# Kernel optimization log

Hardware: AMD Instinct MI355X
Metric: run time of the kernel (lower is better)

The kernel has to match this reference:

```python
import jax, jax.numpy as jnp
import numpy as np

TEMPERATURE = 0.5
EPS = 1e-20


def setup_inputs() -> dict:
    key = jax.random.key(0)
    ks = jax.random.split(key, 7)
    N, T, S = 16, 64, 1024
    SRC, TGT, D = 512, 512, 64
    return {
        "input": jax.random.normal(ks[0], (N, T, TGT), jnp.float32),
        "memory_bank": jax.random.normal(ks[1], (N, S, SRC), jnp.float32),
        "W_q": jax.random.normal(ks[2], (TGT, D), jnp.float32) / np.sqrt(TGT),
        "W_ctx": jax.random.normal(ks[3], (SRC, D), jnp.float32) / np.sqrt(SRC),
        "v": jax.random.normal(ks[4], (D,), jnp.float32) / np.sqrt(D),
        "W_out": jax.random.normal(ks[5], (SRC + TGT, TGT), jnp.float32) / np.sqrt(SRC + TGT),
        "b_out": jax.random.normal(ks[6], (TGT,), jnp.float32) * 0.01,
    }


def reference(input, memory_bank, W_q, W_ctx, v, W_out, b_out):
    # MLP attention score: v^T tanh(W_q q + W_ctx h)
    wq = jnp.einsum("ntd,de->nte", input, W_q)            # [N,T,D]
    uh = jnp.einsum("nsd,de->nse", memory_bank, W_ctx)    # [N,S,D]
    wquh = jnp.tanh(wq[:, :, None, :] + uh[:, None, :, :])  # [N,T,S,D]
    scores = jnp.einsum("ntsd,d->nts", wquh, v)           # [N,T,S]

    log_alpha = jax.nn.log_softmax(scores, axis=-1)
    alpha = jnp.exp(log_alpha)                            # c_align_vectors

    # deterministic context + output
    context_c = jnp.einsum("nts,nsd->ntd", alpha, memory_bank)
    h_c = jnp.tanh(jnp.concatenate([input, context_c], axis=-1) @ W_out + b_out)

    # gumbel-softmax sample (K = n_samples = 1, forced by view_as in original)
    u = jax.random.uniform(jax.random.key(42), log_alpha.shape, jnp.float32)
    g = -jnp.log(-jnp.log(u + EPS) + EPS)                 # gumbel noise
    y_align = jax.nn.softmax((log_alpha + g) / TEMPERATURE, axis=-1)  # [N,T,S]

    context_y = jnp.einsum("nts,nsd->ntd", y_align, memory_bank)
    h_y = jnp.tanh(jnp.concatenate([input, context_y], axis=-1) @ W_out + b_out)

    return jnp.stack([h_c, h_y], axis=0)  # [2,N,T,tgt_dim]
```

## Files before the change

kernel.cpp:

```cpp
#include <hip/hip_runtime.h>
#include <hip/hip_bf16.h>
#include <stdint.h>

#define DEV __device__ __forceinline__

typedef __attribute__((ext_vector_type(8))) short short8;
typedef __attribute__((ext_vector_type(4))) float f32x4;

#define TWO_LOG2E 2.8853900817779268f
#define MFMA16(a, b, c) __builtin_amdgcn_mfma_f32_16x16x32_bf16((a), (b), (c), 0, 0, 0)

DEV unsigned short f2bf(float f) {
  uint32_t u = __float_as_uint(f);
  u += 0x7FFFu + ((u >> 16) & 1u);
  return (unsigned short)(u >> 16);
}

DEV uint2 pk4(float4 f) {
  union { __hip_bfloat162 h; unsigned u; } a, b;
  a.h = __float22bfloat162_rn(make_float2(f.x, f.y));
  b.h = __float22bfloat162_rn(make_float2(f.z, f.w));
  return make_uint2(a.u, b.u);
}

DEV short8 mk8(uint2 lo, uint2 hi) {
  union { short8 s; uint4 u; } t;
  t.u = make_uint4(lo.x, lo.y, hi.x, hi.y);
  return t.s;
}

DEV uint32_t rotl32(uint32_t x, int r) { return (x << r) | (x >> (32 - r)); }

DEV void threefry_0_42(uint32_t x0, uint32_t x1, uint32_t& o0, uint32_t& o1) {
  const uint32_t ks0 = 0u, ks1 = 42u, ks2 = 0x1BD11BDAu ^ 42u;
  x0 += ks0; x1 += ks1;
#define TFR(r) { x0 += x1; x1 = rotl32(x1, (r)); x1 ^= x0; }
  TFR(13) TFR(15) TFR(26) TFR(6)  x0 += ks1; x1 += ks2 + 1u;
  TFR(17) TFR(29) TFR(16) TFR(24) x0 += ks2; x1 += ks0 + 2u;
  TFR(13) TFR(15) TFR(26) TFR(6)  x0 += ks0; x1 += ks1 + 3u;
  TFR(17) TFR(29) TFR(16) TFR(24) x0 += ks1; x1 += ks2 + 4u;
  TFR(13) TFR(15) TFR(26) TFR(6)  x0 += ks2; x1 += ks0 + 5u;
#undef TFR
  o0 = x0; o1 = x1;
}

DEV float wredmax(float v) {
#pragma unroll
  for (int off = 32; off > 0; off >>= 1) v = fmaxf(v, __shfl_xor(v, off));
  return v;
}
DEV float wredsum(float v) {
#pragma unroll
  for (int off = 32; off > 0; off >>= 1) v += __shfl_xor(v, off);
  return v;
}

__global__ __launch_bounds__(256) void k_prep(const float* __restrict__ Wctx,
                                              const float* __restrict__ Wq,
                                              const float* __restrict__ Wout,
                                              unsigned short* __restrict__ WctxT,
                                              unsigned short* __restrict__ WqT,
                                              unsigned short* __restrict__ WoutT) {
  __shared__ float tile[64][65];
  const int b = blockIdx.x;
  const float* src; unsigned short* dst; int R, C, br, bc;
  if (b < 8)       { src = Wctx; dst = WctxT; R = 512;  C = 64;  br = b * 64;       bc = 0; }
  else if (b < 16) { src = Wq;   dst = WqT;   R = 512;  C = 64;  br = (b - 8) * 64; bc = 0; }
  else { int i = b - 16; src = Wout; dst = WoutT; R = 1024; C = 512; br = (i & 15) * 64; bc = (i >> 4) * 64; }
  const int tid = threadIdx.x;
  const int lr = tid >> 4, lc4 = (tid & 15) * 4;
#pragma unroll
  for (int i = 0; i < 4; ++i) {
    float4 vv = *(const float4*)(src + (long)(br + lr + i * 16) * C + bc + lc4);
    tile[lr + i * 16][lc4 + 0] = vv.x;
    tile[lr + i * 16][lc4 + 1] = vv.y;
    tile[lr + i * 16][lc4 + 2] = vv.z;
    tile[lr + i * 16][lc4 + 3] = vv.w;
  }
  __syncthreads();
#pragma unroll
  for (int i = 0; i < 4; ++i) {
    int crow = lr + i * 16;
    ushort4 o;
    o.x = f2bf(tile[lc4 + 0][crow]);
    o.y = f2bf(tile[lc4 + 1][crow]);
    o.z = f2bf(tile[lc4 + 2][crow]);
    o.w = f2bf(tile[lc4 + 3][crow]);
    *(ushort4*)(dst + (long)(bc + crow) * R + br + lc4) = o;
  }
}

__global__ __launch_bounds__(256) void k_gemm1(const float* __restrict__ mb,
                                               const float* __restrict__ input,
                                               const unsigned short* __restrict__ WctxT,
                                               const unsigned short* __restrict__ WqT,
                                               const unsigned short* __restrict__ WoutT,
                                               const float* __restrict__ bout,
                                               float* __restrict__ uhT,
                                               float* __restrict__ wqo,
                                               float* __restrict__ P,
                                               unsigned short* __restrict__ mbT) {
  __shared__ __align__(16) unsigned short As[64][32];
  __shared__ __align__(16) unsigned short Bs[64][32];
  __shared__ __align__(16) unsigned short Tr[32][72];
  const int tid = threadIdx.x;
  const int t = blockIdx.x;
  const int srow = tid >> 2, kc = tid & 3;
  const int scol = ((kc ^ (srow & 3)) * 8);
  const int wave = tid >> 6, lane = tid & 63;
  const int q = lane >> 4, r = lane & 15;
  const int c0 = ((q ^ (r & 3)) * 8);

  if (t < 272) {
    const bool domb = (t < 256);
    const float* A; const unsigned short* BT; int mbase;
    if (domb) { A = mb;    BT = WctxT; mbase = t * 64; }
    else      { A = input; BT = WqT;   mbase = (t - 256) * 64; }
    const int n = mbase >> 10, s0 = mbase & 1023;
    const int wm = (wave >> 1) * 32, wn = (wave & 1) * 32;
    const float* ap = A + (long)(mbase + srow) * 512 + kc * 8;
    const unsigned short* bp = BT + (long)srow * 512 + kc * 8;
    const int trow = tid >> 3, toff = (tid & 7) * 8;
    f32x4 acc[2][2];
#pragma unroll
    for (int i = 0; i < 2; ++i)
#pragma unroll
      for (int j = 0; j < 2; ++j) acc[i][j] = (f32x4){0.f, 0.f, 0.f, 0.f};
    float4 fa0 = *(const float4*)(ap);
    float4 fa1 = *(const float4*)(ap + 4);
    uint4 fb = *(const uint4*)(bp);
    for (int k0 = 0; k0 < 512; k0 += 32) {
      uint2 p0 = pk4(fa0), p1 = pk4(fa1);
      *(uint4*)&As[srow][scol] = make_uint4(p0.x, p0.y, p1.x, p1.y);
      *(uint4*)&Bs[srow][scol] = fb;
      if (domb) {
        const int d0 = kc * 8;
        Tr[d0 + 0][srow] = (unsigned short)(p0.x & 0xFFFFu);
        Tr[d0 + 1][srow] = (unsigned short)(p0.x >> 16);
        Tr[d0 + 2][srow] = (unsigned short)(p0.y & 0xFFFFu);
        Tr[d0 + 3][srow] = (unsigned short)(p0.y >> 16);
        Tr[d0 + 4][srow] = (unsigned short)(p1.x & 0xFFFFu);
        Tr[d0 + 5][srow] = (unsigned short)(p1.x >> 16);
        Tr[d0 + 6][srow] = (unsigned short)(p1.y & 0xFFFFu);
        Tr[d0 + 7][srow] = (unsigned short)(p1.y >> 16);
      }
      __syncthreads();
      if (k0 + 32 < 512) {
        fa0 = *(const float4*)(ap + k0 + 32);
        fa1 = *(const float4*)(ap + k0 + 36);
        fb = *(const uint4*)(bp + k0 + 32);
      }
      short8 a0 = *(const short8*)&As[wm + r][c0];
      short8 a1 = *(const short8*)&As[wm + 16 + r][c0];
      short8 b0 = *(const short8*)&Bs[wn + r][c0];
      short8 b1 = *(const short8*)&Bs[wn + 16 + r][c0];
      acc[0][0] = MFMA16(a0, b0, acc[0][0]);
      acc[0][1] = MFMA16(a0, b1, acc[0][1]);
      acc[1][0] = MFMA16(a1, b0, acc[1][0]);
      acc[1][1] = MFMA16(a1, b1, acc[1][1]);
      if (domb) {
        ushort4 w0 = *(const ushort4*)&Tr[trow][toff];
        ushort4 w1 = *(const ushort4*)&Tr[trow][toff + 4];
        unsigned short* dst = mbT + (long)n * 524288 + (long)(k0 + trow) * 1024 + s0 + toff;
        *(ushort4*)(dst) = w0;
        *(ushort4*)(dst + 4) = w1;
      }
      __syncthreads();
    }
#pragma unroll
    for (int i2 = 0; i2 < 2; ++i2)
#pragma unroll
      for (int j2 = 0; j2 < 2; ++j2) {
        int gcol = wn + j2 * 16 + r;
        int m = mbase + wm + i2 * 16 + q * 4;
        if (domb) {
          int nn = m >> 10, ss = m & 1023;
          float4 o;
          o.x = acc[i2][j2][0] * TWO_LOG2E;
          o.y = acc[i2][j2][1] * TWO_LOG2E;
          o.z = acc[i2][j2][2] * TWO_LOG2E;
          o.w = acc[i2][j2][3] * TWO_LOG2E;
          *(float4*)(uhT + (long)nn * 65536 + (long)gcol * 1024 + ss) = o;
        } else {
#pragma unroll
          for (int reg = 0; reg < 4; ++reg)
            wqo[(long)(m + reg) * 64 + gcol] = acc[i2][j2][reg] * TWO_LOG2E;
        }
      }
  } else {
    const int tt = t - 272;
    const int mbase = (tt >> 4) * 64, nbase = (tt & 15) * 32;
    const int wm = (wave >> 1) * 32, wn = (wave & 1) * 16;
    const float* ap = input + (long)(mbase + srow) * 512 + kc * 8;
    const int brow = (tid & 127) >> 2;
    const unsigned short* bp = WoutT + (long)(nbase + brow) * 1024 + kc * 8;
    f32x4 acc[2];
    acc[0] = (f32x4){0.f, 0.f, 0.f, 0.f};
    acc[1] = (f32x4){0.f, 0.f, 0.f, 0.f};
    float4 fa0 = *(const float4*)(ap);
    float4 fa1 = *(const float4*)(ap + 4);
    uint4 fb;
    if (tid < 128) fb = *(const uint4*)(bp);
    for (int k0 = 0; k0 < 512; k0 += 32) {
      uint2 p0 = pk4(fa0), p1 = pk4(fa1);
      *(uint4*)&As[srow][scol] = make_uint4(p0.x, p0.y, p1.x, p1.y);
      if (tid < 128) *(uint4*)&Bs[brow][(kc ^ (brow & 3)) * 8] = fb;
      __syncthreads();
      int kn = k0 + 32;
      if (kn < 512) {
        fa0 = *(const float4*)(ap + kn);
        fa1 = *(const float4*)(ap + kn + 4);
        if (tid < 128) fb = *(const uint4*)(bp + kn);
      }
      short8 a0 = *(const short8*)&As[wm + r][c0];
      short8 a1 = *(const short8*)&As[wm + 16 + r][c0];
      short8 b0 = *(const short8*)&Bs[wn + r][c0];
      acc[0] = MFMA16(a0, b0, acc[0]);
      acc[1] = MFMA16(a1, b0, acc[1]);
      __syncthreads();
    }
#pragma unroll
    for (int i2 = 0; i2 < 2; ++i2) {
      int gcol = nbase + wn + r;
      float bb = bout[gcol];
#pragma unroll
      for (int reg = 0; reg < 4; ++reg) {
        int grow = mbase + wm + i2 * 16 + q * 4 + reg;
        P[(long)grow * 512 + gcol] = acc[i2][reg] + bb;
      }
    }
  }
}

DEV void softmax_gumbel_write(float* lsc, int nt, int tid, float* red,
                              unsigned short* alpha_bf, unsigned short* yal_bf) {
  const int wv = tid >> 6, ln = tid & 63;
  float m = fmaxf(fmaxf(lsc[0], lsc[1]), fmaxf(lsc[2], lsc[3]));
  m = wredmax(m);
  if (ln == 0) red[wv] = m;
  __syncthreads();
  m = fmaxf(fmaxf(red[0], red[1]), fmaxf(red[2], red[3]));
  __syncthreads();
  float ss = 0.f;
#pragma unroll
  for (int i = 0; i < 4; ++i) ss += __expf(lsc[i] - m);
  ss = wredsum(ss);
  if (ln == 0) red[wv] = ss;
  __syncthreads();
  ss = red[0] + red[1] + red[2] + red[3];
  const float logl = __logf(ss);
  __syncthreads();

  const uint32_t jbase = (uint32_t)nt * 1024u + (uint32_t)tid * 4u;
  float ys[4];
  float4 av;
#pragma unroll
  for (int i = 0; i < 4; ++i) {
    float la = lsc[i] - m - logl;
    ((float*)&av)[i] = __expf(la);
    uint32_t o0, o1;
    threefry_0_42(0u, jbase + i, o0, o1);
    uint32_t bits = o0 ^ o1;
    float u = __uint_as_float((bits >> 9) | 0x3f800000u) - 1.0f;
    float g = -__logf(-__logf(u + 1e-20f) + 1e-20f);
    ys[i] = (la + g) * 2.0f;
  }
  {
    uint2 pa = pk4(av);
    *(uint2*)(alpha_bf + (long)nt * 1024 + tid * 4) = pa;
  }
  float m2 = fmaxf(fmaxf(ys[0], ys[1]), fmaxf(ys[2], ys[3]));
  m2 = wredmax(m2);
  if (ln == 0) red[wv] = m2;
  __syncthreads();
  m2 = fmaxf(fmaxf(red[0], red[1]), fmaxf(red[2], red[3]));
  __syncthreads();
  float s2 = 0.f;
  float4 ye;
#pragma unroll
  for (int i = 0; i < 4; ++i) { ((float*)&ye)[i] = __expf(ys[i] - m2); s2 += ((float*)&ye)[i]; }
  s2 = wredsum(s2);
  if (ln == 0) red[wv] = s2;
  __syncthreads();
  s2 = red[0] + red[1] + red[2] + red[3];
  const float rinv = __fdividef(1.f, s2);
  ye.x *= rinv; ye.y *= rinv; ye.z *= rinv; ye.w *= rinv;
  {
    uint2 py = pk4(ye);
    *(uint2*)(yal_bf + (long)nt * 1024 + tid * 4) = py;
  }
  __syncthreads();
}

__global__ __launch_bounds__(256) void k_scores(const float* __restrict__ uhT,
                                                const float* __restrict__ wqo,
                                                const float* __restrict__ vvec,
                                                unsigned short* __restrict__ alpha_bf,
                                                unsigned short* __restrict__ yal_bf) {
  __shared__ __align__(16) float smf[196];
  float* wvs0 = smf;
  float* wvs1 = smf + 64;
  float* vvs  = smf + 128;
  float* red  = smf + 192;
  const int tid = threadIdx.x;
  const int bid = blockIdx.x;
  const int nt0 = ((bid & 7) << 6) | (bid >> 3);
  const int nt1 = nt0 + 512;
  const int n0 = nt0 >> 6, n1 = nt1 >> 6;
  if (tid < 64) {
    wvs0[tid] = wqo[nt0 * 64 + tid];
    wvs1[tid] = wqo[nt1 * 64 + tid];
    vvs[tid]  = vvec[tid];
  }
  __syncthreads();
  float sumv = 0.f;
#pragma unroll
  for (int d = 0; d < 64; d += 4) {
    float4 vv = *(const float4*)&vvs[d];
    sumv += vv.x + vv.y + vv.z + vv.w;
  }
  const float* un0 = uhT + (long)n0 * 65536 + tid * 4;
  const float* un1 = uhT + (long)n1 * 65536 + tid * 4;
  float4 r0 = make_float4(0.f, 0.f, 0.f, 0.f);
  float4 r1 = make_float4(0.f, 0.f, 0.f, 0.f);
  for (int db = 0; db < 64; db += 4) {
    float4 ua[4], ub[4];
#pragma unroll
    for (int j = 0; j < 4; ++j) {
      ua[j] = *(const float4*)(un0 + (long)(db + j) * 1024);
      ub[j] = *(const float4*)(un1 + (long)(db + j) * 1024);
    }
#pragma unroll
    for (int j = 0; j < 4; ++j) {
      float w0 = wvs0[db + j], w1 = wvs1[db + j], vvj = vvs[db + j];
      r0.x = fmaf(vvj, __builtin_amdgcn_rcpf(1.f + __builtin_amdgcn_exp2f(ua[j].x + w0)), r0.x);
      r0.y = fmaf(vvj, __builtin_amdgcn_rcpf(1.f + __builtin_amdgcn_exp2f(ua[j].y + w0)), r0.y);
      r0.z = fmaf(vvj, __builtin_amdgcn_rcpf(1.f + __builtin_amdgcn_exp2f(ua[j].z + w0)), r0.z);
      r0.w = fmaf(vvj, __builtin_amdgcn_rcpf(1.f + __builtin_amdgcn_exp2f(ua[j].w + w0)), r0.w);
      r1.x = fmaf(vvj, __builtin_amdgcn_rcpf(1.f + __builtin_amdgcn_exp2f(ub[j].x + w1)), r1.x);
      r1.y = fmaf(vvj, __builtin_amdgcn_rcpf(1.f + __builtin_amdgcn_exp2f(ub[j].y + w1)), r1.y);
      r1.z = fmaf(vvj, __builtin_amdgcn_rcpf(1.f + __builtin_amdgcn_exp2f(ub[j].z + w1)), r1.z);
      r1.w = fmaf(vvj, __builtin_amdgcn_rcpf(1.f + __builtin_amdgcn_exp2f(ub[j].w + w1)), r1.w);
    }
  }
  float lsc0[4], lsc1[4];
  lsc0[0] = fmaf(-2.f, r0.x, sumv); lsc0[1] = fmaf(-2.f, r0.y, sumv);
  lsc0[2] = fmaf(-2.f, r0.z, sumv); lsc0[3] = fmaf(-2.f, r0.w, sumv);
  lsc1[0] = fmaf(-2.f, r1.x, sumv); lsc1[1] = fmaf(-2.f, r1.y, sumv);
  lsc1[2] = fmaf(-2.f, r1.z, sumv); lsc1[3] = fmaf(-2.f, r1.w, sumv);
  softmax_gumbel_write(lsc0, nt0, tid, red, alpha_bf, yal_bf);
  softmax_gumbel_write(lsc1, nt1, tid, red, alpha_bf, yal_bf);
}

__global__ __launch_bounds__(256) void k_ctx(const unsigned short* __restrict__ alpha_bf,
                                             const unsigned short* __restrict__ yal_bf,
                                             const unsigned short* __restrict__ mbT,
                                             unsigned short* __restrict__ ctxb) {
  __shared__ __align__(16) unsigned short As[64][32];
  const int tid = threadIdx.x;
  const int x = blockIdx.x;
  const int n = x & 15, dbase = ((x >> 4) & 15) * 32, vt = x >> 8;
  const int srow = tid >> 2, kc = tid & 3;
  const int scol = ((kc ^ (srow & 3)) * 8);
  const int wave = tid >> 6, lane = tid & 63;
  const int wm = (wave >> 1) * 32, wn = (wave & 1) * 16;
  const int q = lane >> 4, r = lane & 15;
  const int c0 = ((q ^ (r & 3)) * 8);
  const unsigned short* Ab = (vt ? yal_bf : alpha_bf) + (long)n * 65536 + (long)srow * 1024 + kc * 8;
  const unsigned short* Bp = mbT + (long)n * 524288 + (long)(dbase + wn + r) * 1024 + q * 8;
  f32x4 acc[2];
  acc[0] = (f32x4){0.f, 0.f, 0.f, 0.f};
  acc[1] = (f32x4){0.f, 0.f, 0.f, 0.f};
  uint4 fa  = *(const uint4*)(Ab);
  uint4 fb0 = *(const uint4*)(Bp);
  uint4 fb1 = *(const uint4*)(Bp + 32);
  for (int k0 = 0; k0 < 1024; k0 += 32) {
    *(uint4*)&As[srow][scol] = fa;
    __syncthreads();
    union { uint4 u; short8 s; } bu; bu.u = fb0;
    if (k0 + 32 < 1024) fa = *(const uint4*)(Ab + k0 + 32);
    fb0 = fb1;
    if (k0 + 64 < 1024) fb1 = *(const uint4*)(Bp + k0 + 64);
    short8 a0 = *(const short8*)&As[wm + r][c0];
    short8 a1 = *(const short8*)&As[wm + 16 + r][c0];
    acc[0] = MFMA16(a0, bu.s, acc[0]);
    acc[1] = MFMA16(a1, bu.s, acc[1]);
    __syncthreads();
  }
#pragma unroll
  for (int i2 = 0; i2 < 2; ++i2) {
    int gcol = dbase + wn + r;
#pragma unroll
    for (int reg = 0; reg < 4; ++reg) {
      long grow = (long)vt * 1024 + n * 64 + wm + i2 * 16 + q * 4 + reg;
      ctxb[grow * 512 + gcol] = f2bf(acc[i2][reg]);
    }
  }
}

__global__ __launch_bounds__(256) void k_out(const unsigned short* __restrict__ ctxb,
                                             const unsigned short* __restrict__ WoutT,
                                             const float* __restrict__ P,
                                             float* __restrict__ out) {
  __shared__ __align__(16) unsigned short As[64][32];
  __shared__ __align__(16) unsigned short Bs[32][32];
  const int tid = threadIdx.x;
  const int mbase = (blockIdx.x >> 4) * 64, nbase = (blockIdx.x & 15) * 32;
  const int srow = tid >> 2, kc = tid & 3;
  const int scol = ((kc ^ (srow & 3)) * 8);
  const int wave = tid >> 6, lane = tid & 63;
  const int wm = (wave >> 1) * 32, wn = (wave & 1) * 16;
  const int q = lane >> 4, r = lane & 15;
  const int c0 = ((q ^ (r & 3)) * 8);
  const unsigned short* ap = ctxb + (long)(mbase + srow) * 512 + kc * 8;
  const int brow = (tid & 127) >> 2;
  const unsigned short* bp = WoutT + (long)(nbase + brow) * 1024 + 512 + kc * 8;
  f32x4 acc[2];
#pragma unroll
  for (int i2 = 0; i2 < 2; ++i2) {
    int pcol = nbase + wn + r;
#pragma unroll
    for (int reg = 0; reg < 4; ++reg) {
      int prow = (mbase + wm + i2 * 16 + q * 4 + reg) & 1023;
      acc[i2][reg] = P[(long)prow * 512 + pcol];
    }
  }
  uint4 fa = *(const uint4*)(ap);
  uint4 fb;
  if (tid < 128) fb = *(const uint4*)(bp);
  for (int k0 = 0; k0 < 512; k0 += 32) {
    *(uint4*)&As[srow][scol] = fa;
    if (tid < 128) *(uint4*)&Bs[brow][(kc ^ (brow & 3)) * 8] = fb;
    __syncthreads();
    int kn = k0 + 32;
    if (kn < 512) {
      fa = *(const uint4*)(ap + kn);
      if (tid < 128) fb = *(const uint4*)(bp + kn);
    }
    short8 a0 = *(const short8*)&As[wm + r][c0];
    short8 a1 = *(const short8*)&As[wm + 16 + r][c0];
    short8 b0 = *(const short8*)&Bs[wn + r][c0];
    acc[0] = MFMA16(a0, b0, acc[0]);
    acc[1] = MFMA16(a1, b0, acc[1]);
    __syncthreads();
  }
#pragma unroll
  for (int i2 = 0; i2 < 2; ++i2) {
    int gcol = nbase + wn + r;
#pragma unroll
    for (int reg = 0; reg < 4; ++reg) {
      int grow = mbase + wm + i2 * 16 + q * 4 + reg;
      float z = acc[i2][reg];
      float rc = __builtin_amdgcn_rcpf(1.f + __builtin_amdgcn_exp2f(z * TWO_LOG2E));
      out[(long)grow * 512 + gcol] = fmaf(-2.f, rc, 1.f);
    }
  }
}

extern "C" void kernel_launch(void* const* d_in, const int* in_sizes, int n_in,
                              void* d_out, int out_size, void* d_ws, size_t ws_size,
                              hipStream_t stream) {
  const float* input = (const float*)d_in[0];
  const float* mb    = (const float*)d_in[1];
  const float* W_q   = (const float*)d_in[2];
  const float* W_ctx = (const float*)d_in[3];
  const float* v     = (const float*)d_in[4];
  const float* W_out = (const float*)d_in[5];
  const float* b_out = (const float*)d_in[6];
  float* out = (float*)d_out;
  float* ws = (float*)d_ws;

  float* uhT = ws;
  float* wqo = ws + 1048576;
  unsigned short* alpha_bf = (unsigned short*)(ws + 1114112);
  unsigned short* yal_bf   = (unsigned short*)(ws + 1638400);
  unsigned short* WctxT = (unsigned short*)(ws + 2162688);
  unsigned short* WqT   = (unsigned short*)(ws + 2179072);
  unsigned short* WoutT = (unsigned short*)(ws + 2195456);
  unsigned short* ctxb  = (unsigned short*)(ws + 2457600);
  float* P = ws + 2981888;
  unsigned short* mbT = (unsigned short*)(ws + 3506176);

  k_prep<<<144, 256, 0, stream>>>(W_ctx, W_q, W_out, WctxT, WqT, WoutT);
  k_gemm1<<<528, 256, 0, stream>>>(mb, input, WctxT, WqT, WoutT, b_out, uhT, wqo, P, mbT);
  k_scores<<<512, 256, 0, stream>>>(uhT, wqo, v, alpha_bf, yal_bf);
  k_ctx<<<512, 256, 0, stream>>>(alpha_bf, yal_bf, mbT, ctxb);
  k_out<<<512, 256, 0, stream>>>(ctxb, WoutT, P, out);
}
```

Measured before the change: 153.1 us.

## Halve per-block tile sizes to double grid size across all GEMM and score kernels

Every kernel is re-tiled so each block handles half as much work: the gemm1 M-tile drops from 64 to 32 rows, k_scores handles one query row per block instead of two, and k_ctx and k_out use 32-row tiles. Grids double from roughly 512 to roughly 1024 blocks, which gives the MI355X's many CUs more blocks to schedule and better latency hiding. In exchange each block reuses less data, so B operands are loaded more often, and half the threads now sit idle during A staging. The transpose tile is reshaped to match, and an unused helper and a trailing barrier are removed.

```diff
diff --git a/kernel.cpp b/kernel.cpp
--- a/kernel.cpp
+++ b/kernel.cpp
@@ -21,12 +21,6 @@
   a.h = __float22bfloat162_rn(make_float2(f.x, f.y));
   b.h = __float22bfloat162_rn(make_float2(f.z, f.w));
   return make_uint2(a.u, b.u);
-}
-
-DEV short8 mk8(uint2 lo, uint2 hi) {
-  union { short8 s; uint4 u; } t;
-  t.u = make_uint4(lo.x, lo.y, hi.x, hi.y);
-  return t.s;
 }
 
 DEV uint32_t rotl32(uint32_t x, int r) { return (x << r) | (x >> (32 - r)); }
@@ -100,134 +94,128 @@
                                                float* __restrict__ wqo,
                                                float* __restrict__ P,
                                                unsigned short* __restrict__ mbT) {
-  __shared__ __align__(16) unsigned short As[64][32];
+  __shared__ __align__(16) unsigned short As[32][32];
   __shared__ __align__(16) unsigned short Bs[64][32];
-  __shared__ __align__(16) unsigned short Tr[32][72];
+  __shared__ __align__(16) unsigned short Tr[32][33];
   const int tid = threadIdx.x;
   const int t = blockIdx.x;
-  const int srow = tid >> 2, kc = tid & 3;
-  const int scol = ((kc ^ (srow & 3)) * 8);
   const int wave = tid >> 6, lane = tid & 63;
   const int q = lane >> 4, r = lane & 15;
   const int c0 = ((q ^ (r & 3)) * 8);
 
-  if (t < 272) {
-    const bool domb = (t < 256);
+  if (t < 544) {
+    const bool domb = (t < 512);
     const float* A; const unsigned short* BT; int mbase;
-    if (domb) { A = mb;    BT = WctxT; mbase = t * 64; }
-    else      { A = input; BT = WqT;   mbase = (t - 256) * 64; }
+    if (domb) { A = mb;    BT = WctxT; mbase = t * 32; }
+    else      { A = input; BT = WqT;   mbase = (t - 512) * 32; }
     const int n = mbase >> 10, s0 = mbase & 1023;
-    const int wm = (wave >> 1) * 32, wn = (wave & 1) * 32;
-    const float* ap = A + (long)(mbase + srow) * 512 + kc * 8;
-    const unsigned short* bp = BT + (long)srow * 512 + kc * 8;
-    const int trow = tid >> 3, toff = (tid & 7) * 8;
-    f32x4 acc[2][2];
-#pragma unroll
-    for (int i = 0; i < 2; ++i)
-#pragma unroll
-      for (int j = 0; j < 2; ++j) acc[i][j] = (f32x4){0.f, 0.f, 0.f, 0.f};
-    float4 fa0 = *(const float4*)(ap);
-    float4 fa1 = *(const float4*)(ap + 4);
-    uint4 fb = *(const uint4*)(bp);
-    for (int k0 = 0; k0 < 512; k0 += 32) {
-      uint2 p0 = pk4(fa0), p1 = pk4(fa1);
-      *(uint4*)&As[srow][scol] = make_uint4(p0.x, p0.y, p1.x, p1.y);
-      *(uint4*)&Bs[srow][scol] = fb;
-      if (domb) {
-        const int d0 = kc * 8;
-        Tr[d0 + 0][srow] = (unsigned short)(p0.x & 0xFFFFu);
-        Tr[d0 + 1][srow] = (unsigned short)(p0.x >> 16);
-        Tr[d0 + 2][srow] = (unsigned short)(p0.y & 0xFFFFu);
-        Tr[d0 + 3][srow] = (unsigned short)(p0.y >> 16);
-        Tr[d0 + 4][srow] = (unsigned short)(p1.x & 0xFFFFu);
-        Tr[d0 + 5][srow] = (unsigned short)(p1.x >> 16);
-        Tr[d0 + 6][srow] = (unsigned short)(p1.y & 0xFFFFu);
-        Tr[d0 + 7][srow] = (unsigned short)(p1.y >> 16);
-      }
-      __syncthreads();
-      if (k0 + 32 < 512) {
-        fa0 = *(const float4*)(ap + k0 + 32);
-        fa1 = *(const float4*)(ap + k0 + 36);
-        fb = *(const uint4*)(bp + k0 + 32);
-      }
-      short8 a0 = *(const short8*)&As[wm + r][c0];
-      short8 a1 = *(const short8*)&As[wm + 16 + r][c0];
-      short8 b0 = *(const short8*)&Bs[wn + r][c0];
-      short8 b1 = *(const short8*)&Bs[wn + 16 + r][c0];
-      acc[0][0] = MFMA16(a0, b0, acc[0][0]);
-      acc[0][1] = MFMA16(a0, b1, acc[0][1]);
-      acc[1][0] = MFMA16(a1, b0, acc[1][0]);
-      acc[1][1] = MFMA16(a1, b1, acc[1][1]);
-      if (domb) {
-        ushort4 w0 = *(const ushort4*)&Tr[trow][toff];
-        ushort4 w1 = *(const ushort4*)&Tr[trow][toff + 4];
-        unsigned short* dst = mbT + (long)n * 524288 + (long)(k0 + trow) * 1024 + s0 + toff;
-        *(ushort4*)(dst) = w0;
-        *(ushort4*)(dst + 4) = w1;
-      }
-      __syncthreads();
-    }
-#pragma unroll
-    for (int i2 = 0; i2 < 2; ++i2)
-#pragma unroll
-      for (int j2 = 0; j2 < 2; ++j2) {
-        int gcol = wn + j2 * 16 + r;
-        int m = mbase + wm + i2 * 16 + q * 4;
-        if (domb) {
-          int nn = m >> 10, ss = m & 1023;
-          float4 o;
-          o.x = acc[i2][j2][0] * TWO_LOG2E;
-          o.y = acc[i2][j2][1] * TWO_LOG2E;
-          o.z = acc[i2][j2][2] * TWO_LOG2E;
-          o.w = acc[i2][j2][3] * TWO_LOG2E;
-          *(float4*)(uhT + (long)nn * 65536 + (long)gcol * 1024 + ss) = o;
-        } else {
-#pragma unroll
-          for (int reg = 0; reg < 4; ++reg)
-            wqo[(long)(m + reg) * 64 + gcol] = acc[i2][j2][reg] * TWO_LOG2E;
-        }
-      }
-  } else {
-    const int tt = t - 272;
-    const int mbase = (tt >> 4) * 64, nbase = (tt & 15) * 32;
-    const int wm = (wave >> 1) * 32, wn = (wave & 1) * 16;
-    const float* ap = input + (long)(mbase + srow) * 512 + kc * 8;
-    const int brow = (tid & 127) >> 2;
-    const unsigned short* bp = WoutT + (long)(nbase + brow) * 1024 + kc * 8;
+    const int wi = wave >> 1, wn = (wave & 1) * 32;
+    const int arow = (tid & 127) >> 2, akc = tid & 3;
+    const int ascol = ((akc ^ (arow & 3)) * 8);
+    const float* ap = A + (long)(mbase + arow) * 512 + akc * 8;
+    const int brow = tid >> 2, bkc = tid & 3;
+    const int bscol = ((bkc ^ (brow & 3)) * 8);
+    const unsigned short* bp = BT + (long)brow * 512 + bkc * 8;
+    const int trow = tid >> 3, toff = (tid & 7) * 4;
     f32x4 acc[2];
     acc[0] = (f32x4){0.f, 0.f, 0.f, 0.f};
     acc[1] = (f32x4){0.f, 0.f, 0.f, 0.f};
-    float4 fa0 = *(const float4*)(ap);
-    float4 fa1 = *(const float4*)(ap + 4);
-    uint4 fb;
-    if (tid < 128) fb = *(const uint4*)(bp);
+    float4 fa0, fa1;
+    if (tid < 128) { fa0 = *(const float4*)(ap); fa1 = *(const float4*)(ap + 4); }
+    uint4 fb = *(const uint4*)(bp);
     for (int k0 = 0; k0 < 512; k0 += 32) {
-      uint2 p0 = pk4(fa0), p1 = pk4(fa1);
-      *(uint4*)&As[srow][scol] = make_uint4(p0.x, p0.y, p1.x, p1.y);
-      if (tid < 128) *(uint4*)&Bs[brow][(kc ^ (brow & 3)) * 8] = fb;
+      if (tid < 128) {
+        uint2 p0 = pk4(fa0), p1 = pk4(fa1);
+        *(uint4*)&As[arow][ascol] = make_uint4(p0.x, p0.y, p1.x, p1.y);
+        if (domb) {
+          const int d0 = akc * 8;
+          Tr[d0 + 0][arow] = (unsigned short)(p0.x & 0xFFFFu);
+          Tr[d0 + 1][arow] = (unsigned short)(p0.x >> 16);
+          Tr[d0 + 2][arow] = (unsigned short)(p0.y & 0xFFFFu);
+          Tr[d0 + 3][arow] = (unsigned short)(p0.y >> 16);
+          Tr[d0 + 4][arow] = (unsigned short)(p1.x & 0xFFFFu);
+          Tr[d0 + 5][arow] = (unsigned short)(p1.x >> 16);
+          Tr[d0 + 6][arow] = (unsigned short)(p1.y & 0xFFFFu);
+          Tr[d0 + 7][arow] = (unsigned short)(p1.y >> 16);
+        }
+      }
+      *(uint4*)&Bs[brow][bscol] = fb;
+      __syncthreads();
+      if (k0 + 32 < 512) {
+        if (tid < 128) {
+          fa0 = *(const float4*)(ap + k0 + 32);
+          fa1 = *(const float4*)(ap + k0 + 36);
+        }
+        fb = *(const uint4*)(bp + k0 + 32);
+      }
+      short8 a0 = *(const short8*)&As[wi * 16 + r][c0];
+      short8 b0 = *(const short8*)&Bs[wn + r][c0];
+      short8 b1 = *(const short8*)&Bs[wn + 16 + r][c0];
+      acc[0] = MFMA16(a0, b0, acc[0]);
+      acc[1] = MFMA16(a0, b1, acc[1]);
+      if (domb) {
+        ushort4 w0 = *(const ushort4*)&Tr[trow][toff];
+        *(ushort4*)(mbT + (long)n * 524288 + (long)(k0 + trow) * 1024 + s0 + toff) = w0;
+      }
+      __syncthreads();
+    }
+#pragma unroll
+    for (int j2 = 0; j2 < 2; ++j2) {
+      int gcol = wn + j2 * 16 + r;
+      int m = mbase + wi * 16 + q * 4;
+      if (domb) {
+        float4 o;
+        o.x = acc[j2][0] * TWO_LOG2E;
+        o.y = acc[j2][1] * TWO_LOG2E;
+        o.z = acc[j2][2] * TWO_LOG2E;
+        o.w = acc[j2][3] * TWO_LOG2E;
+        *(float4*)(uhT + (long)n * 65536 + (long)gcol * 1024 + (m & 1023)) = o;
+      } else {
+#pragma unroll
+        for (int reg = 0; reg < 4; ++reg)
+          wqo[(long)(m + reg) * 64 + gcol] = acc[j2][reg] * TWO_LOG2E;
+      }
+    }
+  } else {
+    const int tt = t - 544;
+    const int mbase = (tt >> 4) * 32, nbase = (tt & 15) * 32;
+    const int wi = wave >> 1, wj = wave & 1;
+    const int arow = (tid & 127) >> 2, akc = tid & 3;
+    const int ascol = ((akc ^ (arow & 3)) * 8);
+    const float* ap = input + (long)(mbase + arow) * 512 + akc * 8;
+    const unsigned short* bp = WoutT + (long)(nbase + arow) * 1024 + akc * 8;
+    f32x4 acc = (f32x4){0.f, 0.f, 0.f, 0.f};
+    float4 fa0, fa1; uint4 fb;
+    if (tid < 128) { fa0 = *(const float4*)(ap); fa1 = *(const float4*)(ap + 4); }
+    else           { fb = *(const uint4*)(bp); }
+    for (int k0 = 0; k0 < 512; k0 += 32) {
+      if (tid < 128) {
+        uint2 p0 = pk4(fa0), p1 = pk4(fa1);
+        *(uint4*)&As[arow][ascol] = make_uint4(p0.x, p0.y, p1.x, p1.y);
+      } else {
+        *(uint4*)&Bs[arow][ascol] = fb;
+      }
       __syncthreads();
       int kn = k0 + 32;
       if (kn < 512) {
-        fa0 = *(const float4*)(ap + kn);
-        fa1 = *(const float4*)(ap + kn + 4);
-        if (tid < 128) fb = *(const uint4*)(bp + kn);
-      }
-      short8 a0 = *(const short8*)&As[wm + r][c0];
-      short8 a1 = *(const short8*)&As[wm + 16 + r][c0];
-      short8 b0 = *(const short8*)&Bs[wn + r][c0];
-      acc[0] = MFMA16(a0, b0, acc[0]);
-      acc[1] = MFMA16(a1, b0, acc[1]);
+        if (tid < 128) {
+          fa0 = *(const float4*)(ap + kn);
+          fa1 = *(const float4*)(ap + kn + 4);
+        } else {
+          fb = *(const uint4*)(bp + kn);
+        }
+      }
+      short8 a0 = *(const short8*)&As[wi * 16 + r][c0];
+      short8 b0 = *(const short8*)&Bs[wj * 16 + r][c0];
+      acc = MFMA16(a0, b0, acc);
       __syncthreads();
     }
-#pragma unroll
-    for (int i2 = 0; i2 < 2; ++i2) {
-      int gcol = nbase + wn + r;
-      float bb = bout[gcol];
-#pragma unroll
-      for (int reg = 0; reg < 4; ++reg) {
-        int grow = mbase + wm + i2 * 16 + q * 4 + reg;
-        P[(long)grow * 512 + gcol] = acc[i2][reg] + bb;
-      }
+    int gcol = nbase + wj * 16 + r;
+    float bb = bout[gcol];
+#pragma unroll
+    for (int reg = 0; reg < 4; ++reg) {
+      int grow = mbase + wi * 16 + q * 4 + reg;
+      P[(long)grow * 512 + gcol] = acc[reg] + bb;
     }
   }
 }
@@ -289,7 +277,6 @@
     uint2 py = pk4(ye);
     *(uint2*)(yal_bf + (long)nt * 1024 + tid * 4) = py;
   }
-  __syncthreads();
 }
 
 __global__ __launch_bounds__(256) void k_scores(const float* __restrict__ uhT,
@@ -297,20 +284,17 @@
                                                 const float* __restrict__ vvec,
                                                 unsigned short* __restrict__ alpha_bf,
                                                 unsigned short* __restrict__ yal_bf) {
-  __shared__ __align__(16) float smf[196];
-  float* wvs0 = smf;
-  float* wvs1 = smf + 64;
-  float* vvs  = smf + 128;
-  float* red  = smf + 192;
+  __shared__ __align__(16) float smf[132];
+  float* wvs = smf;
+  float* vvs = smf + 64;
+  float* red = smf + 128;
   const int tid = threadIdx.x;
   const int bid = blockIdx.x;
-  const int nt0 = ((bid & 7) << 6) | (bid >> 3);
-  const int nt1 = nt0 + 512;
-  const int n0 = nt0 >> 6, n1 = nt1 >> 6;
+  const int nt = ((bid & 7) << 7) | (bid >> 3);
+  const int n = nt >> 6;
   if (tid < 64) {
-    wvs0[tid] = wqo[nt0 * 64 + tid];
-    wvs1[tid] = wqo[nt1 * 64 + tid];
-    vvs[tid]  = vvec[tid];
+    wvs[tid] = wqo[nt * 64 + tid];
+    vvs[tid] = vvec[tid];
   }
   __syncthreads();
   float sumv = 0.f;
@@ -319,82 +303,67 @@
     float4 vv = *(const float4*)&vvs[d];
     sumv += vv.x + vv.y + vv.z + vv.w;
   }
-  const float* un0 = uhT + (long)n0 * 65536 + tid * 4;
-  const float* un1 = uhT + (long)n1 * 65536 + tid * 4;
-  float4 r0 = make_float4(0.f, 0.f, 0.f, 0.f);
-  float4 r1 = make_float4(0.f, 0.f, 0.f, 0.f);
-  for (int db = 0; db < 64; db += 4) {
-    float4 ua[4], ub[4];
-#pragma unroll
-    for (int j = 0; j < 4; ++j) {
-      ua[j] = *(const float4*)(un0 + (long)(db + j) * 1024);
-      ub[j] = *(const float4*)(un1 + (long)(db + j) * 1024);
-    }
-#pragma unroll
-    for (int j = 0; j < 4; ++j) {
-      float w0 = wvs0[db + j], w1 = wvs1[db + j], vvj = vvs[db + j];
-      r0.x = fmaf(vvj, __builtin_amdgcn_rcpf(1.f + __builtin_amdgcn_exp2f(ua[j].x + w0)), r0.x);
-      r0.y = fmaf(vvj, __builtin_amdgcn_rcpf(1.f + __builtin_amdgcn_exp2f(ua[j].y + w0)), r0.y);
-      r0.z = fmaf(vvj, __builtin_amdgcn_rcpf(1.f + __builtin_amdgcn_exp2f(ua[j].z + w0)), r0.z);
-      r0.w = fmaf(vvj, __builtin_amdgcn_rcpf(1.f + __builtin_amdgcn_exp2f(ua[j].w + w0)), r0.w);
-      r1.x = fmaf(vvj, __builtin_amdgcn_rcpf(1.f + __builtin_amdgcn_exp2f(ub[j].x + w1)), r1.x);
-      r1.y = fmaf(vvj, __builtin_amdgcn_rcpf(1.f + __builtin_amdgcn_exp2f(ub[j].y + w1)), r1.y);
-      r1.z = fmaf(vvj, __builtin_amdgcn_rcpf(1.f + __builtin_amdgcn_exp2f(ub[j].z + w1)), r1.z);
-      r1.w = fmaf(vvj, __builtin_amdgcn_rcpf(1.f + __builtin_amdgcn_exp2f(ub[j].w + w1)), r1.w);
-    }
-  }
-  float lsc0[4], lsc1[4];
-  lsc0[0] = fmaf(-2.f, r0.x, sumv); lsc0[1] = fmaf(-2.f, r0.y, sumv);
-  lsc0[2] = fmaf(-2.f, r0.z, sumv); lsc0[3] = fmaf(-2.f, r0.w, sumv);
-  lsc1[0] = fmaf(-2.f, r1.x, sumv); lsc1[1] = fmaf(-2.f, r1.y, sumv);
-  lsc1[2] = fmaf(-2.f, r1.z, sumv); lsc1[3] = fmaf(-2.f, r1.w, sumv);
-  softmax_gumbel_write(lsc0, nt0, tid, red, alpha_bf, yal_bf);
-  softmax_gumbel_write(lsc1, nt1, tid, red, alpha_bf, yal_bf);
+  const float* un = uhT + (long)n * 65536 + tid * 4;
+  float4 racc = make_float4(0.f, 0.f, 0.f, 0.f);
+  for (int db = 0; db < 64; db += 8) {
+    float4 ub[8];
+#pragma unroll
+    for (int j = 0; j < 8; ++j) ub[j] = *(const float4*)(un + (long)(db + j) * 1024);
+#pragma unroll
+    for (int j = 0; j < 8; ++j) {
+      float w = wvs[db + j], vvj = vvs[db + j];
+      racc.x = fmaf(vvj, __builtin_amdgcn_rcpf(1.f + __builtin_amdgcn_exp2f(ub[j].x + w)), racc.x);
+      racc.y = fmaf(vvj, __builtin_amdgcn_rcpf(1.f + __builtin_amdgcn_exp2f(ub[j].y + w)), racc.y);
+      racc.z = fmaf(vvj, __builtin_amdgcn_rcpf(1.f + __builtin_amdgcn_exp2f(ub[j].z + w)), racc.z);
+      racc.w = fmaf(vvj, __builtin_amdgcn_rcpf(1.f + __builtin_amdgcn_exp2f(ub[j].w + w)), racc.w);
+    }
+  }
+  float lsc[4];
+  lsc[0] = fmaf(-2.f, racc.x, sumv);
+  lsc[1] = fmaf(-2.f, racc.y, sumv);
+  lsc[2] = fmaf(-2.f, racc.z, sumv);
+  lsc[3] = fmaf(-2.f, racc.w, sumv);
+  softmax_gumbel_write(lsc, nt, tid, red, alpha_bf, yal_bf);
 }
 
 __global__ __launch_bounds__(256) void k_ctx(const unsigned short* __restrict__ alpha_bf,
                                              const unsigned short* __restrict__ yal_bf,
                                              const unsigned short* __restrict__ mbT,
                                              unsigned short* __restrict__ ctxb) {
-  __shared__ __align__(16) unsigned short As[64][32];
+  __shared__ __align__(16) unsigned short As[32][32];
   const int tid = threadIdx.x;
   const int x = blockIdx.x;
-  const int n = x & 15, dbase = ((x >> 4) & 15) * 32, vt = x >> 8;
-  const int srow = tid >> 2, kc = tid & 3;
-  const int scol = ((kc ^ (srow & 3)) * 8);
+  const int n = x & 15, dbase = ((x >> 4) & 15) * 32, mt = (x >> 8) & 1, vt = x >> 9;
   const int wave = tid >> 6, lane = tid & 63;
-  const int wm = (wave >> 1) * 32, wn = (wave & 1) * 16;
+  const int wi = wave >> 1, wj = wave & 1;
   const int q = lane >> 4, r = lane & 15;
   const int c0 = ((q ^ (r & 3)) * 8);
-  const unsigned short* Ab = (vt ? yal_bf : alpha_bf) + (long)n * 65536 + (long)srow * 1024 + kc * 8;
-  const unsigned short* Bp = mbT + (long)n * 524288 + (long)(dbase + wn + r) * 1024 + q * 8;
-  f32x4 acc[2];
-  acc[0] = (f32x4){0.f, 0.f, 0.f, 0.f};
-  acc[1] = (f32x4){0.f, 0.f, 0.f, 0.f};
-  uint4 fa  = *(const uint4*)(Ab);
+  const int arow = (tid & 127) >> 2, akc = tid & 3;
+  const int ascol = ((akc ^ (arow & 3)) * 8);
+  const unsigned short* ap = (vt ? yal_bf : alpha_bf) + (long)n * 65536
+                             + (long)(mt * 32 + arow) * 1024 + akc * 8;
+  const unsigned short* Bp = mbT + (long)n * 524288 + (long)(dbase + wj * 16 + r) * 1024 + q * 8;
+  f32x4 acc = (f32x4){0.f, 0.f, 0.f, 0.f};
+  uint4 fa;
+  if (tid < 128) fa = *(const uint4*)(ap);
   uint4 fb0 = *(const uint4*)(Bp);
   uint4 fb1 = *(const uint4*)(Bp + 32);
   for (int k0 = 0; k0 < 1024; k0 += 32) {
-    *(uint4*)&As[srow][scol] = fa;
+    if (tid < 128) *(uint4*)&As[arow][ascol] = fa;
     __syncthreads();
     union { uint4 u; short8 s; } bu; bu.u = fb0;
-    if (k0 + 32 < 1024) fa = *(const uint4*)(Ab + k0 + 32);
+    if (k0 + 32 < 1024 && tid < 128) fa = *(const uint4*)(ap + k0 + 32);
     fb0 = fb1;
     if (k0 + 64 < 1024) fb1 = *(const uint4*)(Bp + k0 + 64);
-    short8 a0 = *(const short8*)&As[wm + r][c0];
-    short8 a1 = *(const short8*)&As[wm + 16 + r][c0];
-    acc[0] = MFMA16(a0, bu.s, acc[0]);
-    acc[1] = MFMA16(a1, bu.s, acc[1]);
+    short8 a0 = *(const short8*)&As[wi * 16 + r][c0];
+    acc = MFMA16(a0, bu.s, acc);
     __syncthreads();
   }
-#pragma unroll
-  for (int i2 = 0; i2 < 2; ++i2) {
-    int gcol = dbase + wn + r;
-#pragma unroll
-    for (int reg = 0; reg < 4; ++reg) {
-      long grow = (long)vt * 1024 + n * 64 + wm + i2 * 16 + q * 4 + reg;
-      ctxb[grow * 512 + gcol] = f2bf(acc[i2][reg]);
-    }
+  int gcol = dbase + wj * 16 + r;
+#pragma unroll
+  for (int reg = 0; reg < 4; ++reg) {
+    long grow = (long)vt * 1024 + n * 64 + mt * 32 + wi * 16 + q * 4 + reg;
+    ctxb[grow * 512 + gcol] = f2bf(acc[reg]);
   }
 }
 
@@ -402,58 +371,51 @@
                                              const unsigned short* __restrict__ WoutT,
                                              const float* __restrict__ P,
                                              float* __restrict__ out) {
-  __shared__ __align__(16) unsigned short As[64][32];
+  __shared__ __align__(16) unsigned short As[32][32];
   __shared__ __align__(16) unsigned short Bs[32][32];
   const int tid = threadIdx.x;
-  const int mbase = (blockIdx.x >> 4) * 64, nbase = (blockIdx.x & 15) * 32;
-  const int srow = tid >> 2, kc = tid & 3;
-  const int scol = ((kc ^ (srow & 3)) * 8);
+  const int mbase = (blockIdx.x >> 4) * 32, nbase = (blockIdx.x & 15) * 32;
   const int wave = tid >> 6, lane = tid & 63;
-  const int wm = (wave >> 1) * 32, wn = (wave & 1) * 16;
+  const int wi = wave >> 1, wj = wave & 1;
   const int q = lane >> 4, r = lane & 15;
   const int c0 = ((q ^ (r & 3)) * 8);
-  const unsigned short* ap = ctxb + (long)(mbase + srow) * 512 + kc * 8;
-  const int brow = (tid & 127) >> 2;
-  const unsigned short* bp = WoutT + (long)(nbase + brow) * 1024 + 512 + kc * 8;
-  f32x4 acc[2];
-#pragma unroll
-  for (int i2 = 0; i2 < 2; ++i2) {
-    int pcol = nbase + wn + r;
+  const int arow = (tid & 127) >> 2, akc = tid & 3;
+  const int ascol = ((akc ^ (arow & 3)) * 8);
+  const unsigned short* ap = ctxb + (long)(mbase + arow) * 512 + akc * 8;
+  const unsigned short* bp = WoutT + (long)(nbase + arow) * 1024 + 512 + akc * 8;
+  f32x4 acc;
+  {
+    int pcol = nbase + wj * 16 + r;
 #pragma unroll
     for (int reg = 0; reg < 4; ++reg) {
-      int prow = (mbase + wm + i2 * 16 + q * 4 + reg) & 1023;
-      acc[i2][reg] = P[(long)prow * 512 + pcol];
-    }
-  }
-  uint4 fa = *(const uint4*)(ap);
-  uint4 fb;
-  if (tid < 128) fb = *(const uint4*)(bp);
+      int prow = (mbase + wi * 16 + q * 4 + reg) & 1023;
+      acc[reg] = P[(long)prow * 512 + pcol];
+    }
+  }
+  uint4 fa, fb;
+  if (tid < 128) fa = *(const uint4*)(ap);
+  else           fb = *(const uint4*)(bp);
   for (int k0 = 0; k0 < 512; k0 += 32) {
-    *(uint4*)&As[srow][scol] = fa;
-    if (tid < 128) *(uint4*)&Bs[brow][(kc ^ (brow & 3)) * 8] = fb;
+    if (tid < 128) *(uint4*)&As[arow][ascol] = fa;
+    else           *(uint4*)&Bs[arow][ascol] = fb;
     __syncthreads();
     int kn = k0 + 32;
     if (kn < 512) {
-      fa = *(const uint4*)(ap + kn);
-      if (tid < 128) fb = *(const uint4*)(bp + kn);
-    }
-    short8 a0 = *(const short8*)&As[wm + r][c0];
-    short8 a1 = *(const short8*)&As[wm + 16 + r][c0];
-    short8 b0 = *(const short8*)&Bs[wn + r][c0];
-    acc[0] = MFMA16(a0, b0, acc[0]);
-    acc[1] = MFMA16(a1, b0, acc[1]);
+      if (tid < 128) fa = *(const uint4*)(ap + kn);
+      else           fb = *(const uint4*)(bp + kn);
+    }
+    short8 a0 = *(const short8*)&As[wi * 16 + r][c0];
+    short8 b0 = *(const short8*)&Bs[wj * 16 + r][c0];
+    acc = MFMA16(a0, b0, acc);
     __syncthreads();
   }
-#pragma unroll
-  for (int i2 = 0; i2 < 2; ++i2) {
-    int gcol = nbase + wn + r;
-#pragma unroll
-    for (int reg = 0; reg < 4; ++reg) {
-      int grow = mbase + wm + i2 * 16 + q * 4 + reg;
-      float z = acc[i2][reg];
-      float rc = __builtin_amdgcn_rcpf(1.f + __builtin_amdgcn_exp2f(z * TWO_LOG2E));
-      out[(long)grow * 512 + gcol] = fmaf(-2.f, rc, 1.f);
-    }
+  int gcol = nbase + wj * 16 + r;
+#pragma unroll
+  for (int reg = 0; reg < 4; ++reg) {
+    int grow = mbase + wi * 16 + q * 4 + reg;
+    float z = acc[reg];
+    float rc = __builtin_amdgcn_rcpf(1.f + __builtin_amdgcn_exp2f(z * TWO_LOG2E));
+    out[(long)grow * 512 + gcol] = fmaf(-2.f, rc, 1.f);
   }
 }
 
@@ -482,8 +444,8 @@
   unsigned short* mbT = (unsigned short*)(ws + 3506176);
 
   k_prep<<<144, 256, 0, stream>>>(W_ctx, W_q, W_out, WctxT, WqT, WoutT);
-  k_gemm1<<<528, 256, 0, stream>>>(mb, input, WctxT, WqT, WoutT, b_out, uhT, wqo, P, mbT);
-  k_scores<<<512, 256, 0, stream>>>(uhT, wqo, v, alpha_bf, yal_bf);
-  k_ctx<<<512, 256, 0, stream>>>(alpha_bf, yal_bf, mbT, ctxb);
-  k_out<<<512, 256, 0, stream>>>(ctxb, WoutT, P, out);
-}
+  k_gemm1<<<1056, 256, 0, stream>>>(mb, input, WctxT, WqT, WoutT, b_out, uhT, wqo, P, mbT);
+  k_scores<<<1024, 256, 0, stream>>>(uhT, wqo, v, alpha_bf, yal_bf);
+  k_ctx<<<1024, 256, 0, stream>>>(alpha_bf, yal_bf, mbT, ctxb);
+  k_out<<<1024, 256, 0, stream>>>(ctxb, WoutT, P, out);
+}
```

New measurement: 151.6 us. About the same (-1.0%).
